# Kernel optimization log

Hardware: AMD Instinct MI355X
Metric: run time of the kernel (lower is better)

Reference implementation:

```python
import jax, jax.numpy as jnp
import numpy as np

# Config matching init_kwargs / input_specs
B, S = 8, 1024          # sequences, uniform seq_len (cu_seqlens = arange*S)
H, KVH, D = 32, 8, 128  # GQA: 4 query heads per kv head
BS, BPB, NB = 16, 64, 512  # block_size, blocks per seq, total blocks
T = B * S
SCALE = 0.08838834764831845  # 1/sqrt(head_dim)


def setup_inputs() -> dict:
    key = jax.random.key(0)
    kq, kk, kv = jax.random.split(key, 3)
    q = jax.random.normal(kq, (T, H * D), dtype=jnp.float32)
    k = jax.random.normal(kk, (T, KVH * D), dtype=jnp.float32)
    v = jax.random.normal(kv, (T, KVH * D), dtype=jnp.float32)
    k_cache = jnp.zeros((NB, BS, KVH, D), dtype=jnp.float32)
    v_cache = jnp.zeros((NB, BS, KVH, D), dtype=jnp.float32)
    # Contiguous page assignment: seq b uses blocks [b*BPB, (b+1)*BPB)
    block_tables = jnp.arange(B * BPB, dtype=jnp.int32).reshape(B, BPB)
    # token (b, t) -> slot block_tables[b, t//BS]*BS + t%BS == global arange here
    slot_mapping = jnp.arange(T, dtype=jnp.int32)
    return {"q": q, "k": k, "v": v, "k_cache": k_cache, "v_cache": v_cache,
            "slot_mapping": slot_mapping, "block_tables": block_tables}


def reference(q, k, v, k_cache, v_cache, slot_mapping, block_tables):
    # [T, H*D] -> [T, H, D]
    q = q.reshape(T, H, D)
    k = k.reshape(T, KVH, D)
    v = v.reshape(T, KVH, D)

    # store_kvcache: scatter new K/V into paged cache via slot_mapping
    kc = k_cache.reshape(NB * BS, KVH, D).at[slot_mapping].set(k)
    vc = v_cache.reshape(NB * BS, KVH, D).at[slot_mapping].set(v)

    # gather pages per sequence: [B, BPB, BS, KVH, D] -> [B, S, KVH, D]
    kg = kc.reshape(NB, BS, KVH, D)[block_tables].reshape(B, S, KVH, D)
    vg = vc.reshape(NB, BS, KVH, D)[block_tables].reshape(B, S, KVH, D)

    # GQA: expand kv heads to query heads
    G = H // KVH
    kg = jnp.repeat(kg, G, axis=2)  # [B, S, H, D]
    vg = jnp.repeat(vg, G, axis=2)

    qb = q.reshape(B, S, H, D)
    scores = jnp.einsum('bqhd,bkhd->bhqk', qb, kg) * SCALE  # [B, H, S, S]
    causal = jnp.tril(jnp.ones((S, S), dtype=bool))
    scores = jnp.where(causal[None, None], scores, jnp.finfo(scores.dtype).min)
    probs = jax.nn.softmax(scores, axis=-1)
    o = jnp.einsum('bhqk,bkhd->bqhd', probs, vg)  # [B, S, H, D]
    return o.reshape(T, H * D)
```

## Files before the change

kernel.cpp:

```cpp
#include <hip/hip_runtime.h>
#include <hip/hip_bf16.h>


namespace {

constexpr int Bc = 8, Sc = 1024, Hc = 32, KVHc = 8, Dc = 128;
constexpr float SCALEc = 0.08838834764831845f;
constexpr int KVBLK = 64;
constexpr int KD = KVHc * Dc;
constexpr int HD = Hc * Dc;
constexpr int NT = 17;

typedef __attribute__((ext_vector_type(8))) short bf16x8;
typedef __attribute__((ext_vector_type(16))) float f32x16;

__device__ __forceinline__ unsigned short f2bf(float f) {
  union { __hip_bfloat16 h; unsigned short u; } c;
  c.h = __float2bfloat16(f);
  return c.u;
}
__device__ __forceinline__ unsigned pack2(float a, float b) {
  return (unsigned)f2bf(a) | ((unsigned)f2bf(b) << 16);
}
__device__ __forceinline__ void pl32swap(unsigned& a, unsigned& b) {
  asm volatile("v_permlane32_swap_b32 %0, %1" : "+v"(a), "+v"(b));
}

template <int ST>
__device__ __forceinline__ f32x16 qk_sub(const unsigned short* KB,
                                         const bf16x8* qf, int q32, int hi) {
  f32x16 a;
#pragma unroll
  for (int i = 0; i < 16; ++i) a[i] = 0.f;
  const int key = ST * 32 + q32;
  const char* kb = (const char*)KB + key * 256;
  const int sw = (key & 15) << 4;
#pragma unroll
  for (int ks = 0; ks < 8; ++ks) {
    bf16x8 kf = *(const bf16x8*)(kb + ((ks * 32 + hi * 16) ^ sw));
    a = __builtin_amdgcn_mfma_f32_32x32x16_bf16(kf, qf[ks], a, 0, 0, 0);
  }
  return a;
}

template <int ST>
__device__ __forceinline__ void pv_sub(const unsigned short* VB,
                                       const f32x16& p, f32x16* acc,
                                       int q32, int hi) {
  unsigned cp[8];
#pragma unroll
  for (int j = 0; j < 8; ++j) cp[j] = pack2(p[2 * j], p[2 * j + 1]);
  pl32swap(cp[0], cp[2]);
  pl32swap(cp[1], cp[3]);
  pl32swap(cp[4], cp[6]);
  pl32swap(cp[5], cp[7]);
  union { bf16x8 v; unsigned u[4]; } f0, f1;
  f0.u[0] = cp[0]; f0.u[1] = cp[1]; f0.u[2] = cp[2]; f0.u[3] = cp[3];
  f1.u[0] = cp[4]; f1.u[1] = cp[5]; f1.u[2] = cp[6]; f1.u[3] = cp[7];
#pragma unroll
  for (int ks2 = 0; ks2 < 2; ++ks2) {
    const bf16x8 pa = ks2 ? f1.v : f0.v;
#pragma unroll
    for (int dt = 0; dt < 4; ++dt) {
      const int d = dt * 32 + q32;
      const bf16x8 vf = *(const bf16x8*)(
          (const char*)VB + d * 128 +
          ((ST * 64 + ks2 * 32 + hi * 16) ^ ((d & 7) << 4)));
      acc[dt] = __builtin_amdgcn_mfma_f32_32x32x16_bf16(vf, pa, acc[dt], 0, 0, 0);
    }
  }
}

__global__ __launch_bounds__(512, 2) void attn_fwd(
    const float* __restrict__ qg, const float* __restrict__ kg,
    const float* __restrict__ vg, float* __restrict__ out) {
  const int bid = blockIdx.x;
  const int j   = bid >> 6;
  const int kvh = bid & 7;
  const int b   = (bid >> 3) & 7;
  const int nA  = 16 - j;

  const int tid = threadIdx.x;
  const int w = tid >> 6, l = tid & 63;
  const int q32 = l & 31, hi = l >> 5;
  const int h = kvh * 4 + (w >> 1);
  const int stdiag = w & 1;

  int qbase = (15 - j) * 64 + (w & 1) * 32;

  __shared__ unsigned short Kl[2][KVBLK * Dc];
  __shared__ unsigned short Vt[2][Dc * KVBLK];

  bf16x8 qf[8];
  auto LOADQ = [&](int qb_) {
    const float* qp = qg + (size_t)(b * Sc + qb_ + q32) * HD + h * Dc;
#pragma unroll
    for (int ks = 0; ks < 8; ++ks) {
      const int d0 = ks * 16 + hi * 8;
      float4 x = *(const float4*)(qp + d0);
      float4 y = *(const float4*)(qp + d0 + 4);
      bf16x8 t;
      t[0] = (short)f2bf(x.x * SCALEc); t[1] = (short)f2bf(x.y * SCALEc);
      t[2] = (short)f2bf(x.z * SCALEc); t[3] = (short)f2bf(x.w * SCALEc);
      t[4] = (short)f2bf(y.x * SCALEc); t[5] = (short)f2bf(y.y * SCALEc);
      t[6] = (short)f2bf(y.z * SCALEc); t[7] = (short)f2bf(y.w * SCALEc);
      qf[ks] = t;
    }
  };
  LOADQ(qbase);

  f32x16 acc[4];
#pragma unroll
  for (int dt = 0; dt < 4; ++dt)
#pragma unroll
    for (int i = 0; i < 16; ++i) acc[dt][i] = 0.f;
  float m = -1e30f, lsum = 0.f;

  auto WRITEO = [&](int qb_) {
    const float rinv = 1.0f / lsum;
    float* ob = out + (size_t)(b * Sc + qb_ + q32) * HD + h * Dc;
#pragma unroll
    for (int dt = 0; dt < 4; ++dt)
#pragma unroll
      for (int g = 0; g < 4; ++g) {
        float4 o;
        o.x = acc[dt][g * 4 + 0] * rinv;
        o.y = acc[dt][g * 4 + 1] * rinv;
        o.z = acc[dt][g * 4 + 2] * rinv;
        o.w = acc[dt][g * 4 + 3] * rinv;
        *(float4*)(ob + dt * 32 + g * 8 + hi * 4) = o;
      }
  };

  const float* kb0 = kg + (size_t)(b * Sc) * KD + kvh * Dc;
  const float* vb0 = vg + (size_t)(b * Sc) * KD + kvh * Dc;

  const int krow = tid >> 3, kd0 = (tid & 7) * 16;
  const int vd = tid & 127, vk0 = (tid >> 7) * 16;

  float4 kreg[4];
  float vreg[16];

  auto LOAD = [&](int T) {
    const float* kp = kb0 + ((size_t)T * KVBLK + krow) * KD + kd0;
    kreg[0] = *(const float4*)(kp);
    kreg[1] = *(const float4*)(kp + 4);
    kreg[2] = *(const float4*)(kp + 8);
    kreg[3] = *(const float4*)(kp + 12);
    const float* vp = vb0 + ((size_t)T * KVBLK + vk0) * KD + vd;
#pragma unroll
    for (int jj = 0; jj < 16; ++jj) vreg[jj] = vp[(size_t)jj * KD];
  };
  auto STORE = [&](int cb) {
    unsigned short* KB = Kl[cb];
    unsigned short* VB = Vt[cb];
    uint4 A, Bq;
    A.x = pack2(kreg[0].x, kreg[0].y); A.y = pack2(kreg[0].z, kreg[0].w);
    A.z = pack2(kreg[1].x, kreg[1].y); A.w = pack2(kreg[1].z, kreg[1].w);
    Bq.x = pack2(kreg[2].x, kreg[2].y); Bq.y = pack2(kreg[2].z, kreg[2].w);
    Bq.z = pack2(kreg[3].x, kreg[3].y); Bq.w = pack2(kreg[3].z, kreg[3].w);
    const int kbase = krow * 256, ksw = (krow & 15) << 4;
    *(uint4*)((char*)KB + kbase + ((kd0 * 2) ^ ksw)) = A;
    *(uint4*)((char*)KB + kbase + ((kd0 * 2 + 16) ^ ksw)) = Bq;
    uint4 C0, C1;
    C0.x = pack2(vreg[0], vreg[1]);   C0.y = pack2(vreg[2], vreg[3]);
    C0.z = pack2(vreg[4], vreg[5]);   C0.w = pack2(vreg[6], vreg[7]);
    C1.x = pack2(vreg[8], vreg[9]);   C1.y = pack2(vreg[10], vreg[11]);
    C1.z = pack2(vreg[12], vreg[13]); C1.w = pack2(vreg[14], vreg[15]);
    const int vbase = vd * 128, vsw = (vd & 7) << 4;
    *(uint4*)((char*)VB + vbase + ((vk0 * 2) ^ vsw)) = C0;
    *(uint4*)((char*)VB + vbase + ((vk0 * 2 + 16) ^ vsw)) = C1;
  };
  auto KT = [&](int i) { return i < nA ? i : i - nA; };

  LOAD(0);
  STORE(0);
  LOAD(KT(1));
  __syncthreads();

  for (int i = 0; i < NT; ++i) {
    const int cb = i & 1;
    if (i + 1 < NT) {
      STORE(cb ^ 1);
      if (i + 2 < NT) LOAD(KT(i + 2));
    }
    if (i == nA) {
      WRITEO(qbase);
      qbase = j * 64 + (w & 1) * 32;
      LOADQ(qbase);
#pragma unroll
      for (int dt = 0; dt < 4; ++dt)
#pragma unroll
        for (int z = 0; z < 16; ++z) acc[dt][z] = 0.f;
      m = -1e30f;
      lsum = 0.f;
    }
    const int kt = KT(i);
    const unsigned short* KB = Kl[cb];
    const unsigned short* VB = Vt[cb];
    const bool last = (i == nA - 1) || (i == NT - 1);
    const bool has1 = !(last && stdiag == 0);

    __builtin_amdgcn_s_setprio(1);
    f32x16 p0 = qk_sub<0>(KB, qf, q32, hi);
    f32x16 p1;
    if (has1) {
      p1 = qk_sub<1>(KB, qf, q32, hi);
    } else {
#pragma unroll
      for (int i2 = 0; i2 < 16; ++i2) p1[i2] = -1e30f;
    }
    __builtin_amdgcn_s_setprio(0);

    if (last) {
      const int kmb = kt * KVBLK + stdiag * 32 + 4 * hi - qbase - q32;
      if (stdiag == 0) {
#pragma unroll
        for (int i2 = 0; i2 < 16; ++i2) {
          const int kl = (i2 & 3) + 8 * (i2 >> 2);
          if (kmb + kl > 0) p0[i2] = -1e30f;
        }
      } else {
#pragma unroll
        for (int i2 = 0; i2 < 16; ++i2) {
          const int kl = (i2 & 3) + 8 * (i2 >> 2);
          if (kmb + kl > 0) p1[i2] = -1e30f;
        }
      }
    }

    float pm = fmaxf(p0[0], p1[0]);
#pragma unroll
    for (int i2 = 1; i2 < 16; ++i2) pm = fmaxf(pm, fmaxf(p0[i2], p1[i2]));
    pm = fmaxf(pm, __shfl_xor(pm, 32));
    if (__any(pm > m + 8.0f)) {
      const float mn = fmaxf(m, pm);
      const float alpha = __expf(m - mn);
      m = mn;
      lsum *= alpha;
#pragma unroll
      for (int dt = 0; dt < 4; ++dt) acc[dt] *= alpha;
    }
    float se = 0.f;
#pragma unroll
    for (int i2 = 0; i2 < 16; ++i2) { p0[i2] = __expf(p0[i2] - m); se += p0[i2]; }
    if (has1) {
#pragma unroll
      for (int i2 = 0; i2 < 16; ++i2) { p1[i2] = __expf(p1[i2] - m); se += p1[i2]; }
    }
    se += __shfl_xor(se, 32);
    lsum += se;

    __builtin_amdgcn_s_setprio(1);
    pv_sub<0>(VB, p0, acc, q32, hi);
    if (has1) pv_sub<1>(VB, p1, acc, q32, hi);
    __builtin_amdgcn_s_setprio(0);

    __syncthreads();
  }

  WRITEO(qbase);
}

}

extern "C" void kernel_launch(void* const* d_in, const int* in_sizes, int n_in,
                              void* d_out, int out_size, void* d_ws, size_t ws_size,
                              hipStream_t stream) {
  const float* q = (const float*)d_in[0];
  const float* k = (const float*)d_in[1];
  const float* v = (const float*)d_in[2];
  float* out = (float*)d_out;
  dim3 grid(512);
  attn_fwd<<<grid, dim3(512), 0, stream>>>(q, k, v, out);
}
```

Baseline: 155.3 us.

## Software-pipeline QK of next tile with softmax/PV of previous tile

Restructures the main loop so each iteration computes QK scores for tile i while finishing softmax and PV for tile i-1. K/V LDS buffers go from double to triple buffering to hold the extra stage. Launch bounds drop from 2 to 1 block per CU to free registers for the carried score tiles. The goal is to overlap exp/softmax VALU work with MFMA work, at the cost of lower occupancy and more LDS.

```diff
diff --git a/kernel.cpp b/kernel.cpp
--- a/kernel.cpp
+++ b/kernel.cpp
@@ -71,7 +71,7 @@
   }
 }
 
-__global__ __launch_bounds__(512, 2) void attn_fwd(
+__global__ __launch_bounds__(512, 1) void attn_fwd(
     const float* __restrict__ qg, const float* __restrict__ kg,
     const float* __restrict__ vg, float* __restrict__ out) {
   const int bid = blockIdx.x;
@@ -88,8 +88,8 @@
 
   int qbase = (15 - j) * 64 + (w & 1) * 32;
 
-  __shared__ unsigned short Kl[2][KVBLK * Dc];
-  __shared__ unsigned short Vt[2][Dc * KVBLK];
+  __shared__ unsigned short Kl[3][KVBLK * Dc];
+  __shared__ unsigned short Vt[3][Dc * KVBLK];
 
   bf16x8 qf[8];
   auto LOADQ = [&](int qb_) {
@@ -173,21 +173,114 @@
   };
   auto KT = [&](int i) { return i < nA ? i : i - nA; };
 
+  f32x16 s0, s1;
+  bool has1p = true;
+  float alphaSave = 1.f;
+  bool doRescale = false;
+
+  auto MASK = [&](int i, f32x16& p0, f32x16& p1) {
+    const int kt = KT(i);
+    const int kmb = kt * KVBLK + stdiag * 32 + 4 * hi - qbase - q32;
+    if (stdiag == 0) {
+#pragma unroll
+      for (int z = 0; z < 16; ++z) {
+        const int kl = (z & 3) + 8 * (z >> 2);
+        if (kmb + kl > 0) p0[z] = -1e30f;
+      }
+    } else {
+#pragma unroll
+      for (int z = 0; z < 16; ++z) {
+        const int kl = (z & 3) + 8 * (z >> 2);
+        if (kmb + kl > 0) p1[z] = -1e30f;
+      }
+    }
+  };
+  auto MAXMERGE = [&](const f32x16& p0, const f32x16& p1, bool has1) {
+    float pm = p0[0];
+#pragma unroll
+    for (int z = 1; z < 16; ++z) pm = fmaxf(pm, p0[z]);
+    if (has1) {
+#pragma unroll
+      for (int z = 0; z < 16; ++z) pm = fmaxf(pm, p1[z]);
+    }
+    pm = fmaxf(pm, __shfl_xor(pm, 32));
+    if (__any(pm > m + 8.0f)) {
+      const float mn = fmaxf(m, pm);
+      alphaSave = __expf(m - mn);
+      m = mn;
+      doRescale = true;
+    } else {
+      doRescale = false;
+    }
+  };
+  auto FINISH_PV = [&](const unsigned short* VB) {
+    if (doRescale) {
+      lsum *= alphaSave;
+#pragma unroll
+      for (int dt = 0; dt < 4; ++dt) acc[dt] *= alphaSave;
+    }
+    float se = 0.f;
+#pragma unroll
+    for (int z = 0; z < 16; ++z) { s0[z] = __expf(s0[z] - m); se += s0[z]; }
+    if (has1p) {
+#pragma unroll
+      for (int z = 0; z < 16; ++z) { s1[z] = __expf(s1[z] - m); se += s1[z]; }
+    }
+    se += __shfl_xor(se, 32);
+    lsum += se;
+    __builtin_amdgcn_s_setprio(1);
+    pv_sub<0>(VB, s0, acc, q32, hi);
+    if (has1p) pv_sub<1>(VB, s1, acc, q32, hi);
+    __builtin_amdgcn_s_setprio(0);
+  };
+
   LOAD(0);
   STORE(0);
   LOAD(KT(1));
   __syncthreads();
 
-  for (int i = 0; i < NT; ++i) {
-    const int cb = i & 1;
-    if (i + 1 < NT) {
-      STORE(cb ^ 1);
-      if (i + 2 < NT) LOAD(KT(i + 2));
-    }
-    if (i == nA) {
-      WRITEO(qbase);
+  {
+    STORE(1);
+    LOAD(KT(2));
+    f32x16 p0, p1;
+    __builtin_amdgcn_s_setprio(1);
+    p0 = qk_sub<0>(Kl[0], qf, q32, hi);
+    p1 = qk_sub<1>(Kl[0], qf, q32, hi);
+    __builtin_amdgcn_s_setprio(0);
+    MAXMERGE(p0, p1, true);
+    s0 = p0; s1 = p1; has1p = true;
+    __syncthreads();
+  }
+
+  for (int i = 1; i < NT; ++i) {
+    if (i + 1 < NT) STORE((i + 1) % 3);
+    if (i + 2 < NT) LOAD(KT(i + 2));
+
+    int qsave = qbase;
+    const bool sw = (i == nA);
+    if (sw) {
       qbase = j * 64 + (w & 1) * 32;
       LOADQ(qbase);
+    }
+
+    const bool last = (i == nA - 1) || (i == NT - 1);
+    const bool has1 = !(last && stdiag == 0);
+    f32x16 p0, p1;
+    __builtin_amdgcn_s_setprio(1);
+    p0 = qk_sub<0>(Kl[i % 3], qf, q32, hi);
+    if (has1) {
+      p1 = qk_sub<1>(Kl[i % 3], qf, q32, hi);
+    } else {
+#pragma unroll
+      for (int z = 0; z < 16; ++z) p1[z] = -1e30f;
+    }
+    __builtin_amdgcn_s_setprio(0);
+    if (last) MASK(i, p0, p1);
+
+    FINISH_PV(Vt[(i - 1) % 3]);
+
+    if (sw) {
+      WRITEO(qsave);
 #pragma unroll
       for (int dt = 0; dt < 4; ++dt)
 #pragma unroll
@@ -195,70 +288,13 @@
       m = -1e30f;
       lsum = 0.f;
     }
-    const int kt = KT(i);
-    const unsigned short* KB = Kl[cb];
-    const unsigned short* VB = Vt[cb];
-    const bool last = (i == nA - 1) || (i == NT - 1);
-    const bool has1 = !(last && stdiag == 0);
-
-    __builtin_amdgcn_s_setprio(1);
-    f32x16 p0 = qk_sub<0>(KB, qf, q32, hi);
-    f32x16 p1;
-    if (has1) {
-      p1 = qk_sub<1>(KB, qf, q32, hi);
-    } else {
-#pragma unroll
-      for (int i2 = 0; i2 < 16; ++i2) p1[i2] = -1e30f;
-    }
-    __builtin_amdgcn_s_setprio(0);
-
-    if (last) {
-      const int kmb = kt * KVBLK + stdiag * 32 + 4 * hi - qbase - q32;
-      if (stdiag == 0) {
-#pragma unroll
-        for (int i2 = 0; i2 < 16; ++i2) {
-          const int kl = (i2 & 3) + 8 * (i2 >> 2);
-          if (kmb + kl > 0) p0[i2] = -1e30f;
-        }
-      } else {
-#pragma unroll
-        for (int i2 = 0; i2 < 16; ++i2) {
-          const int kl = (i2 & 3) + 8 * (i2 >> 2);
-          if (kmb + kl > 0) p1[i2] = -1e30f;
-        }
-      }
-    }
-
-    float pm = fmaxf(p0[0], p1[0]);
-#pragma unroll
-    for (int i2 = 1; i2 < 16; ++i2) pm = fmaxf(pm, fmaxf(p0[i2], p1[i2]));
-    pm = fmaxf(pm, __shfl_xor(pm, 32));
-    if (__any(pm > m + 8.0f)) {
-      const float mn = fmaxf(m, pm);
-      const float alpha = __expf(m - mn);
-      m = mn;
-      lsum *= alpha;
-#pragma unroll
-      for (int dt = 0; dt < 4; ++dt) acc[dt] *= alpha;
-    }
-    float se = 0.f;
-#pragma unroll
-    for (int i2 = 0; i2 < 16; ++i2) { p0[i2] = __expf(p0[i2] - m); se += p0[i2]; }
-    if (has1) {
-#pragma unroll
-      for (int i2 = 0; i2 < 16; ++i2) { p1[i2] = __expf(p1[i2] - m); se += p1[i2]; }
-    }
-    se += __shfl_xor(se, 32);
-    lsum += se;
-
-    __builtin_amdgcn_s_setprio(1);
-    pv_sub<0>(VB, p0, acc, q32, hi);
-    if (has1) pv_sub<1>(VB, p1, acc, q32, hi);
-    __builtin_amdgcn_s_setprio(0);
-
+
+    MAXMERGE(p0, p1, has1);
+    s0 = p0; s1 = p1; has1p = has1;
     __syncthreads();
   }
 
+  FINISH_PV(Vt[(NT - 1) % 3]);
   WRITEO(qbase);
 }
 
```

Result: slower. 256.1 us (+64.9%).
